# Optimization experiments

Measured on AMD Instinct MI355X. Metric: run time of the kernel, lower is better.

Reference implementation:

```python
import jax, jax.numpy as jnp
import numpy as np

NDIM = (256, 256, 256)
NMIN = (-1.0, -1.0, -1.0)
NMAX = (1.0, 1.0, 1.0)
NDELTA = tuple((NMAX[i] - NMIN[i]) / (NDIM[i] - 1.0) for i in range(3))
MIN_DEG, MAX_DEG = 0, 10
ANNEALED_ALPHA = 1.0
EPS = 1e-12


def compute_grad(grid):
    # central differences on the voxel grid with edge padding -> [N, 3]
    g = grid.reshape(NDIM[0], NDIM[1], NDIM[2])
    p = jnp.pad(g, ((1, 1), (1, 1), (1, 1)), mode='edge')
    dx = (p[2:, 1:-1, 1:-1] - p[:-2, 1:-1, 1:-1]) / (2.0 * NDELTA[0])
    dy = (p[1:-1, 2:, 1:-1] - p[1:-1, :-2, 1:-1]) / (2.0 * NDELTA[1])
    dz = (p[1:-1, 1:-1, 2:] - p[1:-1, 1:-1, :-2]) / (2.0 * NDELTA[2])
    return jnp.stack([dx, dy, dz], axis=-1).reshape(-1, 3)


def trilinear3(data, pts):
    # data: [N, 4] flattened voxel features, pts: [B, 3] -> [B, 4]
    x = (pts[..., 0] - NMIN[0]) / NDELTA[0]
    y = (pts[..., 1] - NMIN[1]) / NDELTA[1]
    z = (pts[..., 2] - NMIN[2]) / NDELTA[2]
    x0f = jnp.floor(x); y0f = jnp.floor(y); z0f = jnp.floor(z)
    xd = (x - x0f)[..., None]
    yd = (y - y0f)[..., None]
    zd = (z - z0f)[..., None]
    x0 = jnp.clip(x0f.astype(jnp.int32), 0, NDIM[0] - 1)
    x1 = jnp.clip(x0f.astype(jnp.int32) + 1, 0, NDIM[0] - 1)
    y0 = jnp.clip(y0f.astype(jnp.int32), 0, NDIM[1] - 1)
    y1 = jnp.clip(y0f.astype(jnp.int32) + 1, 0, NDIM[1] - 1)
    z0 = jnp.clip(z0f.astype(jnp.int32), 0, NDIM[2] - 1)
    z1 = jnp.clip(z0f.astype(jnp.int32) + 1, 0, NDIM[2] - 1)
    sYZ, sZ = NDIM[1] * NDIM[2], NDIM[2]
    gat = lambda i, j, k: data[sYZ * i + sZ * j + k]
    c00 = gat(x0, y0, z0) * (1 - xd) + gat(x1, y0, z0) * xd
    c01 = gat(x0, y0, z1) * (1 - xd) + gat(x1, y0, z1) * xd
    c10 = gat(x0, y1, z0) * (1 - xd) + gat(x1, y1, z0) * xd
    c11 = gat(x0, y1, z1) * (1 - xd) + gat(x1, y1, z1) * xd
    c0 = c00 * (1 - yd) + c10 * yd
    c1 = c01 * (1 - yd) + c11 * yd
    return c0 * (1 - zd) + c1 * zd


def annealed_pos_enc(x, alpha):
    # nerfies-style windowed positional encoding with identity concat
    bands = jnp.arange(MIN_DEG, MAX_DEG, dtype=x.dtype)  # [D]
    scales = 2.0 ** bands
    xb = x[..., None, :] * scales[:, None]               # [..., D, 3]
    four = jnp.sin(jnp.stack([xb, xb + 0.5 * jnp.pi], axis=-2))  # [..., D, 2, 3]
    w = jnp.clip(alpha - bands, 0.0, 1.0)
    w = 0.5 * (1.0 - jnp.cos(jnp.pi * w))                # cosine easing window
    four = four * w[:, None, None]
    four = four.reshape(x.shape[:-1] + (-1,))            # [..., D*6]
    return jnp.concatenate([x, four], axis=-1)           # [..., 3 + D*6]


def mlp(feats, w0, b0, w1, b1, w2, b2, w3, b3, wo, bo):
    # net_depth=4, skip_layer=2 -> concat inputs after layer index 2
    h = jax.nn.relu(feats @ w0 + b0)
    h = jax.nn.relu(h @ w1 + b1)
    h = jax.nn.relu(h @ w2 + b2)
    h = jnp.concatenate([h, feats], axis=-1)
    h = jax.nn.relu(h @ w3 + b3)
    return h @ wo + bo


def safe_l2_norm(v):
    return jnp.sqrt(jnp.sum(v * v, axis=-1, keepdims=True) + EPS)


def setup_inputs() -> dict:
    key = jax.random.key(0)
    ks = jax.random.split(key, 8)
    B = 1048576
    N = NDIM[0] * NDIM[1] * NDIM[2]
    x = jax.random.uniform(ks[0], (B, 3), jnp.float32, -1.0, 1.0)
    grid = jax.random.normal(ks[1], (N, 1), jnp.float32)
    glorot = lambda k, fi, fo: jax.random.normal(k, (fi, fo), jnp.float32) * jnp.sqrt(2.0 / (fi + fo))
    return {
        'x': x, 'grid': grid,
        'w0': glorot(ks[2], 63, 128), 'b0': jnp.zeros((128,), jnp.float32),
        'w1': glorot(ks[3], 128, 128), 'b1': jnp.zeros((128,), jnp.float32),
        'w2': glorot(ks[4], 128, 128), 'b2': jnp.zeros((128,), jnp.float32),
        'w3': glorot(ks[5], 191, 128), 'b3': jnp.zeros((128,), jnp.float32),
        'wo': jax.random.normal(ks[6], (128, 3), jnp.float32) * 1e-5,  # output_init normal(1e-5)
        'bo': jnp.zeros((3,), jnp.float32),
    }


def reference(x, grid, w0, b0, w1, b1, w2, b2, w3, b3, wo, bo):
    data = jnp.concatenate([grid, compute_grad(grid)], axis=-1)  # [N, 4]
    ret = trilinear3(data, x)                                    # [B, 4]
    feats = annealed_pos_enc(x[:, None], ANNEALED_ALPHA * MAX_DEG)  # [B, 1, 63]
    raw = mlp(feats, w0, b0, w1, b1, w2, b2, w3, b3, wo, bo)[:, 0]  # [B, 3]
    # residual + direct output: rotate gradient vector by axis-angle raw
    theta = safe_l2_norm(raw)
    e = raw / theta
    cond = ret[..., 1:]
    a = safe_l2_norm(cond)
    v = cond / a
    rot = a * (jnp.cos(theta) * v + jnp.sin(theta) * jnp.cross(e, v)
               + (1.0 - jnp.cos(theta)) * jnp.sum(e * v, axis=-1, keepdims=True) * e)
    return (ret[..., :1], ret[..., 1:], rot)
```

## Files before the change

### kernel.cpp

```cpp
#include <hip/hip_runtime.h>


typedef __attribute__((ext_vector_type(4))) float f4;
typedef long long llg;

__device__ __forceinline__ float bf2f(unsigned int u) {
    union { float f; unsigned int i; } v; v.i = u << 16; return v.f;
}
__device__ __forceinline__ unsigned int pkbf(float a, float b) {
    unsigned int r;
    asm("v_cvt_pk_bf16_f32 %0, %1, %2" : "=v"(r) : "v"(a), "v"(b));
    return r;
}
__device__ __forceinline__ float gv(const float* __restrict__ g, int i, int j, int k) {
    return g[(i * 256 + j) * 256 + k];
}
__device__ __forceinline__ int featmap(int kp) {
    if (kp < 3) return kp;
    if (kp == 3) return -1;
    const int m = kp - 4, b = m / 6, r = m - 6 * b, d = r >> 1, c = r & 1;
    return 3 + 6 * b + 3 * c + d;
}
__device__ __forceinline__ int hidperm(int k) {
    const int kt = k >> 5, q = (k >> 3) & 3, j = k & 7;
    return 32 * kt + ((j >> 2) << 4) + (q << 2) + (j & 3);
}
__device__ __forceinline__ llg mkllg(unsigned int lo, unsigned int hi) {
    return (llg)(((unsigned long long)lo) | (((unsigned long long)hi) << 32));
}
__device__ __forceinline__ unsigned int pack8(f4 acc) {
    int d = __builtin_amdgcn_cvt_pk_fp8_f32(fmaxf(acc[0], 0.f), fmaxf(acc[1], 0.f), 0, false);
    d     = __builtin_amdgcn_cvt_pk_fp8_f32(fmaxf(acc[2], 0.f), fmaxf(acc[3], 0.f), d, true);
    return (unsigned int)d;
}

#define WS_TOTAL 67584
#define SWZ_BLOCKS 264
#define DG_BLOCKS 8192
#define DG_OFF_SH 131072
#define WS_NEED (262144ull + 16777216ull * 8ull)
#define WO_SCALE 8192.0f
#define WO_INV   (1.0f / 8192.0f)

__global__ __launch_bounds__(256) void prep(
    const float* __restrict__ g,
    const float* __restrict__ w0, const float* __restrict__ w1,
    const float* __restrict__ w2, const float* __restrict__ w3,
    const float* __restrict__ wo,
    unsigned char* __restrict__ ws8, unsigned short* __restrict__ dg,
    int do_dgrid)
{
    const int bid = blockIdx.x;
    if (bid < SWZ_BLOCKS) {
        int idx = bid * 256 + threadIdx.x;
        const float* src; int base, NT, Kact, Nact, ld;
        if (idx < 8192)       { src = w0; base = 0;     NT = 8; Kact = 64;  Nact = 128; ld = 128; }
        else if (idx < 24576) { src = w1; base = 8192;  NT = 8; Kact = 128; Nact = 128; ld = 128; }
        else if (idx < 40960) { src = w2; base = 24576; NT = 8; Kact = 128; Nact = 128; ld = 128; }
        else if (idx < 65536) { src = w3; base = 40960; NT = 8; Kact = 192; Nact = 128; ld = 128; }
        else                  { src = wo; base = 65536; NT = 1; Kact = 128; Nact = 3;   ld = 3;   }
        int local = idx - base;
        int j = local & 7;
        int lane = (local >> 3) & 63;
        int chunk = local >> 9;
        int nt = chunk % NT, kt = chunk / NT;
        int k = kt * 32 + ((lane >> 4) << 3) + j;
        int n = nt * 16 + (lane & 15);
        float v = 0.0f;
        if (k < Kact && n < Nact) {
            int ko;
            if (base == 0) {
                ko = featmap(k);
            } else if (base == 40960) {
                if (k >= 128) {
                    int f = featmap(k - 128);
                    ko = (f < 0) ? -1 : 128 + f;
                } else {
                    ko = hidperm(k);
                }
            } else {
                ko = hidperm(k);
            }
            if (ko >= 0) v = src[ko * ld + n];
            if (base == 65536) v *= WO_SCALE;
        }
        int p = __builtin_amdgcn_cvt_pk_fp8_f32(v, v, 0, false);
        ws8[idx] = (unsigned char)(p & 0xff);
    } else if (do_dgrid) {
        const int t  = (bid - SWZ_BLOCKS) * 256 + threadIdx.x;
        const int k0 = (t & 31) << 3;
        const int j  = (t >> 5) & 255;
        const int i  = t >> 13;
        const float* row = g + (i * 256 + j) * 256;
        const float* rxp = g + (min(i + 1, 255) * 256 + j) * 256;
        const float* rxm = g + (max(i - 1, 0)   * 256 + j) * 256;
        const float* ryp = g + (i * 256 + min(j + 1, 255)) * 256;
        const float* rym = g + (i * 256 + max(j - 1, 0))   * 256;
        float se[8], sxp[8], sxm[8], syp[8], sym[8];
        {
            f4 a = *(const f4*)(row + k0), b = *(const f4*)(row + k0 + 4);
            #pragma unroll
            for (int q = 0; q < 4; ++q) { se[q] = a[q]; se[q + 4] = b[q]; }
            a = *(const f4*)(rxp + k0); b = *(const f4*)(rxp + k0 + 4);
            #pragma unroll
            for (int q = 0; q < 4; ++q) { sxp[q] = a[q]; sxp[q + 4] = b[q]; }
            a = *(const f4*)(rxm + k0); b = *(const f4*)(rxm + k0 + 4);
            #pragma unroll
            for (int q = 0; q < 4; ++q) { sxm[q] = a[q]; sxm[q + 4] = b[q]; }
            a = *(const f4*)(ryp + k0); b = *(const f4*)(ryp + k0 + 4);
            #pragma unroll
            for (int q = 0; q < 4; ++q) { syp[q] = a[q]; syp[q + 4] = b[q]; }
            a = *(const f4*)(rym + k0); b = *(const f4*)(rym + k0 + 4);
            #pragma unroll
            for (int q = 0; q < 4; ++q) { sym[q] = a[q]; sym[q + 4] = b[q]; }
        }
        float zv[10];
        zv[0] = row[max(k0 - 1, 0)];
        #pragma unroll
        for (int q = 0; q < 8; ++q) zv[q + 1] = se[q];
        zv[9] = row[min(k0 + 8, 255)];
        unsigned int o[16];
        #pragma unroll
        for (int q = 0; q < 8; ++q) {
            o[q * 2 + 0] = pkbf(se[q], (sxp[q] - sxm[q]) * 63.75f);
            o[q * 2 + 1] = pkbf((syp[q] - sym[q]) * 63.75f, (zv[q + 2] - zv[q]) * 63.75f);
        }
        unsigned short* dst = dg + (size_t)(((i * 256 + j) * 256 + k0)) * 4;
        #pragma unroll
        for (int q = 0; q < 4; ++q)
            *(uint4*)(dst + q * 8) = *(const uint4*)(&o[q * 4]);
    }
}

#define FSTRIDE_B 88
#define WV_BYTES (32 * FSTRIDE_B)

#define HIDDEN_LAYER(WSL, BIASP, SRC, DST)                                     \
    do {                                                                       \
        _Pragma("unroll")                                                      \
        for (int ut = 0; ut < 8; ++ut) {                                       \
            llg wf0 = *(const llg*)((WSL) + (((0 * 8 + ut) * 64 + lane) << 3));\
            llg wf1 = *(const llg*)((WSL) + (((1 * 8 + ut) * 64 + lane) << 3));\
            llg wf2 = *(const llg*)((WSL) + (((2 * 8 + ut) * 64 + lane) << 3));\
            llg wf3 = *(const llg*)((WSL) + (((3 * 8 + ut) * 64 + lane) << 3));\
            const f4 bias = *(const f4*)((BIASP) + ut * 16 + quad * 4);        \
            _Pragma("unroll")                                                  \
            for (int pt = 0; pt < 2; ++pt) {                                   \
                f4 acc = bias;                                                 \
                acc = __builtin_amdgcn_mfma_f32_16x16x32_fp8_fp8(              \
                        wf0, mkllg(SRC[pt][0], SRC[pt][1]), acc, 0, 0, 0);     \
                acc = __builtin_amdgcn_mfma_f32_16x16x32_fp8_fp8(              \
                        wf1, mkllg(SRC[pt][2], SRC[pt][3]), acc, 0, 0, 0);     \
                acc = __builtin_amdgcn_mfma_f32_16x16x32_fp8_fp8(              \
                        wf2, mkllg(SRC[pt][4], SRC[pt][5]), acc, 0, 0, 0);     \
                acc = __builtin_amdgcn_mfma_f32_16x16x32_fp8_fp8(              \
                        wf3, mkllg(SRC[pt][6], SRC[pt][7]), acc, 0, 0, 0);     \
                DST[pt][ut] = pack8(acc);                                      \
            }                                                                  \
        }                                                                      \
    } while (0)

template<bool FAST>
__global__ __launch_bounds__(256, 5) void voxmlp(
    const float* __restrict__ x, const float* __restrict__ grid,
    const unsigned char* __restrict__ ws8, const unsigned short* __restrict__ dg,
    const float* __restrict__ b0, const float* __restrict__ b1,
    const float* __restrict__ b2, const float* __restrict__ b3,
    const float* __restrict__ bo,
    float* __restrict__ out, int B)
{
    __shared__ unsigned char smem[WV_BYTES * 4];

    const int lane = threadIdx.x & 63;
    const int wave = threadIdx.x >> 6;
    const int quad = lane >> 4;
    const int lm   = lane & 15;
    unsigned char* fbuf = smem + wave * WV_BYTES;

    const int pbase = blockIdx.x * 128 + wave * 32;

    const int p2   = lane & 31;
    const int role = lane >> 5;
    const int pid  = pbase + p2;

    const float px = x[pid * 3 + 0];
    const float py = x[pid * 3 + 1];
    const float pz = x[pid * 3 + 2];

    if (role == 0) {
        const float fx = (px + 1.0f) * 127.5f;
        const float fy = (py + 1.0f) * 127.5f;
        const float fz = (pz + 1.0f) * 127.5f;
        const float fx0 = floorf(fx), fy0 = floorf(fy), fz0 = floorf(fz);
        const float xd = fx - fx0, yd = fy - fy0, zd = fz - fz0;
        const int ix0 = min(max((int)fx0, 0), 255);
        const int iy0 = min(max((int)fy0, 0), 255);
        const int iz0 = min(max((int)fz0, 0), 255);
        const int ix1 = min(ix0 + 1, 255);
        const int iy1 = min(iy0 + 1, 255);
        const int iz1 = min(iz0 + 1, 255);

        float ret0 = 0.f, c1 = 0.f, c2 = 0.f, c3 = 0.f;
        if (FAST) {
            #pragma unroll
            for (int c = 0; c < 8; ++c) {
                const int i = (c & 4) ? ix1 : ix0;
                const int j = (c & 2) ? iy1 : iy0;
                const int k = (c & 1) ? iz1 : iz0;
                const float wgt = ((c & 4) ? xd : 1.0f - xd) *
                                  ((c & 2) ? yd : 1.0f - yd) *
                                  ((c & 1) ? zd : 1.0f - zd);
                const uint2 w = *(const uint2*)(dg + (size_t)((i * 256 + j) * 256 + k) * 4);
                ret0 = fmaf(wgt, bf2f(w.x & 0xffffu), ret0);
                c1   = fmaf(wgt, bf2f(w.x >> 16),     c1);
                c2   = fmaf(wgt, bf2f(w.y & 0xffffu), c2);
                c3   = fmaf(wgt, bf2f(w.y >> 16),     c3);
            }
        } else {
            #pragma unroll
            for (int c = 0; c < 8; ++c) {
                const int i = (c & 4) ? ix1 : ix0;
                const int j = (c & 2) ? iy1 : iy0;
                const int k = (c & 1) ? iz1 : iz0;
                const float wgt = ((c & 4) ? xd : 1.0f - xd) *
                                  ((c & 2) ? yd : 1.0f - yd) *
                                  ((c & 1) ? zd : 1.0f - zd);
                const float v  = gv(grid, i, j, k);
                const float gx = (gv(grid, min(i + 1, 255), j, k) - gv(grid, max(i - 1, 0), j, k)) * 63.75f;
                const float gy = (gv(grid, i, min(j + 1, 255), k) - gv(grid, i, max(j - 1, 0), k)) * 63.75f;
                const float gz = (gv(grid, i, j, min(k + 1, 255)) - gv(grid, i, j, max(k - 1, 0))) * 63.75f;
                ret0 = fmaf(wgt, v,  ret0);
                c1   = fmaf(wgt, gx, c1);
                c2   = fmaf(wgt, gy, c2);
                c3   = fmaf(wgt, gz, c3);
            }
        }
        out[pid] = ret0;
        out[B + pid * 3 + 0] = c1;
        out[B + pid * 3 + 1] = c2;
        out[B + pid * 3 + 2] = c3;
        float* cst = (float*)(fbuf + p2 * FSTRIDE_B + 64);
        cst[0] = c1; cst[1] = c2; cst[2] = c3;
    } else {
        float s[64];
        s[0] = px; s[1] = py; s[2] = pz; s[3] = 0.0f;
        const float crd[3] = {px, py, pz};
        float sc = 1.0f;
        #pragma unroll
        for (int b = 0; b < 10; ++b) {
            #pragma unroll
            for (int d = 0; d < 3; ++d) {
                float sv, cv;
                __sincosf(crd[d] * sc, &sv, &cv);
                s[4 + b * 6 + d * 2 + 0] = sv;
                s[4 + b * 6 + d * 2 + 1] = cv;
            }
            sc *= 2.0f;
        }
        unsigned int dw[16];
        #pragma unroll
        for (int i = 0; i < 16; ++i) {
            int d = __builtin_amdgcn_cvt_pk_fp8_f32(s[4 * i + 0], s[4 * i + 1], 0, false);
            d     = __builtin_amdgcn_cvt_pk_fp8_f32(s[4 * i + 2], s[4 * i + 3], d, true);
            dw[i] = (unsigned int)d;
        }
        unsigned char* fb = fbuf + p2 * FSTRIDE_B;
        #pragma unroll
        for (int i = 0; i < 8; ++i) {
            uint2 pk; pk.x = dw[2 * i]; pk.y = dw[2 * i + 1];
            *(uint2*)(fb + i * 8) = pk;
        }
    }
    __builtin_amdgcn_s_barrier();

    const int frow0 = lm * FSTRIDE_B + quad * 8;

    unsigned int actA[2][8];
    unsigned int actB[2][8];

    {
        llg ff[2][2];
        #pragma unroll
        for (int pt = 0; pt < 2; ++pt)
            #pragma unroll
            for (int kt = 0; kt < 2; ++kt)
                ff[pt][kt] = *(const llg*)(fbuf + pt * 16 * FSTRIDE_B + frow0 + kt * 32);
        #pragma unroll
        for (int ut = 0; ut < 8; ++ut) {
            llg wf0 = *(const llg*)(ws8 + (((0 * 8 + ut) * 64 + lane) << 3));
            llg wf1 = *(const llg*)(ws8 + (((1 * 8 + ut) * 64 + lane) << 3));
            const f4 bias = *(const f4*)(b0 + ut * 16 + quad * 4);
            #pragma unroll
            for (int pt = 0; pt < 2; ++pt) {
                f4 acc = bias;
                acc = __builtin_amdgcn_mfma_f32_16x16x32_fp8_fp8(wf0, ff[pt][0], acc, 0, 0, 0);
                acc = __builtin_amdgcn_mfma_f32_16x16x32_fp8_fp8(wf1, ff[pt][1], acc, 0, 0, 0);
                actA[pt][ut] = pack8(acc);
            }
        }
    }

    HIDDEN_LAYER(ws8 + 8192,  b1, actA, actB);
    HIDDEN_LAYER(ws8 + 24576, b2, actB, actA);

    {
        llg ff[2][2];
        #pragma unroll
        for (int pt = 0; pt < 2; ++pt)
            #pragma unroll
            for (int kk = 0; kk < 2; ++kk)
                ff[pt][kk] = *(const llg*)(fbuf + pt * 16 * FSTRIDE_B + frow0 + kk * 32);
        #pragma unroll
        for (int ut = 0; ut < 8; ++ut) {
            llg wf0 = *(const llg*)(ws8 + 40960 + (((0 * 8 + ut) * 64 + lane) << 3));
            llg wf1 = *(const llg*)(ws8 + 40960 + (((1 * 8 + ut) * 64 + lane) << 3));
            llg wf2 = *(const llg*)(ws8 + 40960 + (((2 * 8 + ut) * 64 + lane) << 3));
            llg wf3 = *(const llg*)(ws8 + 40960 + (((3 * 8 + ut) * 64 + lane) << 3));
            llg wf4 = *(const llg*)(ws8 + 40960 + (((4 * 8 + ut) * 64 + lane) << 3));
            llg wf5 = *(const llg*)(ws8 + 40960 + (((5 * 8 + ut) * 64 + lane) << 3));
            const f4 bias = *(const f4*)(b3 + ut * 16 + quad * 4);
            #pragma unroll
            for (int pt = 0; pt < 2; ++pt) {
                f4 acc = bias;
                acc = __builtin_amdgcn_mfma_f32_16x16x32_fp8_fp8(
                        wf0, mkllg(actA[pt][0], actA[pt][1]), acc, 0, 0, 0);
                acc = __builtin_amdgcn_mfma_f32_16x16x32_fp8_fp8(
                        wf1, mkllg(actA[pt][2], actA[pt][3]), acc, 0, 0, 0);
                acc = __builtin_amdgcn_mfma_f32_16x16x32_fp8_fp8(
                        wf2, mkllg(actA[pt][4], actA[pt][5]), acc, 0, 0, 0);
                acc = __builtin_amdgcn_mfma_f32_16x16x32_fp8_fp8(
                        wf3, mkllg(actA[pt][6], actA[pt][7]), acc, 0, 0, 0);
                acc = __builtin_amdgcn_mfma_f32_16x16x32_fp8_fp8(wf4, ff[pt][0], acc, 0, 0, 0);
                acc = __builtin_amdgcn_mfma_f32_16x16x32_fp8_fp8(wf5, ff[pt][1], acc, 0, 0, 0);
                actB[pt][ut] = pack8(acc);
            }
        }
    }

    llg wf0 = *(const llg*)(ws8 + 65536 + ((0 * 64 + lane) << 3));
    llg wf1 = *(const llg*)(ws8 + 65536 + ((1 * 64 + lane) << 3));
    llg wf2 = *(const llg*)(ws8 + 65536 + ((2 * 64 + lane) << 3));
    llg wf3 = *(const llg*)(ws8 + 65536 + ((3 * 64 + lane) << 3));

    const float bo0 = bo[0], bo1 = bo[1], bo2 = bo[2];
    #pragma unroll
    for (int pt = 0; pt < 2; ++pt) {
        f4 acc = {0.f, 0.f, 0.f, 0.f};
        acc = __builtin_amdgcn_mfma_f32_16x16x32_fp8_fp8(
                wf0, mkllg(actB[pt][0], actB[pt][1]), acc, 0, 0, 0);
        acc = __builtin_amdgcn_mfma_f32_16x16x32_fp8_fp8(
                wf1, mkllg(actB[pt][2], actB[pt][3]), acc, 0, 0, 0);
        acc = __builtin_amdgcn_mfma_f32_16x16x32_fp8_fp8(
                wf2, mkllg(actB[pt][4], actB[pt][5]), acc, 0, 0, 0);
        acc = __builtin_amdgcn_mfma_f32_16x16x32_fp8_fp8(
                wf3, mkllg(actB[pt][6], actB[pt][7]), acc, 0, 0, 0);

        const int pp = pt * 16 + lm;
        const float* cst = (const float*)(fbuf + pp * FSTRIDE_B + 64);
        const float g1 = cst[0], g2 = cst[1], g3 = cst[2];
        const float r0 = acc[0] * WO_INV + bo0;
        const float r1 = acc[1] * WO_INV + bo1;
        const float r2 = acc[2] * WO_INV + bo2;
        const float theta = sqrtf(fmaf(r0, r0, fmaf(r1, r1, r2 * r2)) + 1e-12f);
        const float it = __builtin_amdgcn_rcpf(theta);
        const float e0 = r0 * it, e1 = r1 * it, e2 = r2 * it;
        const float a = sqrtf(fmaf(g1, g1, fmaf(g2, g2, g3 * g3)) + 1e-12f);
        const float ia = __builtin_amdgcn_rcpf(a);
        const float v0 = g1 * ia, v1 = g2 * ia, v2 = g3 * ia;
        float st, ct;
        __sincosf(theta, &st, &ct);
        const float cx = e1 * v2 - e2 * v1;
        const float cy = e2 * v0 - e0 * v2;
        const float cz = e0 * v1 - e1 * v0;
        const float om = (1.0f - ct) * (e0 * v0 + e1 * v1 + e2 * v2);
        if (quad == 0) {
            const int pid2 = pbase + pp;
            out[4 * B + pid2 * 3 + 0] = a * (ct * v0 + st * cx + om * e0);
            out[4 * B + pid2 * 3 + 1] = a * (ct * v1 + st * cy + om * e1);
            out[4 * B + pid2 * 3 + 2] = a * (ct * v2 + st * cz + om * e2);
        }
    }
}

extern "C" void kernel_launch(void* const* d_in, const int* in_sizes, int n_in,
                              void* d_out, int out_size, void* d_ws, size_t ws_size,
                              hipStream_t stream)
{
    const float* x    = (const float*)d_in[0];
    const float* grid = (const float*)d_in[1];
    const float* w0   = (const float*)d_in[2];
    const float* b0   = (const float*)d_in[3];
    const float* w1   = (const float*)d_in[4];
    const float* b1   = (const float*)d_in[5];
    const float* w2   = (const float*)d_in[6];
    const float* b2   = (const float*)d_in[7];
    const float* w3   = (const float*)d_in[8];
    const float* b3   = (const float*)d_in[9];
    const float* wo   = (const float*)d_in[10];
    const float* bo   = (const float*)d_in[11];
    float* out = (float*)d_out;
    unsigned char* ws8 = (unsigned char*)d_ws;
    unsigned short* dg = (unsigned short*)d_ws + DG_OFF_SH;

    const int B = in_sizes[0] / 3;
    const int fast = (ws_size >= WS_NEED) ? 1 : 0;
    const int nprep = fast ? (SWZ_BLOCKS + DG_BLOCKS) : SWZ_BLOCKS;
    prep<<<nprep, 256, 0, stream>>>(grid, w0, w1, w2, w3, wo, ws8, dg, fast);
    if (fast)
        voxmlp<true><<<B / 128, 256, 0, stream>>>(x, grid, ws8, dg, b0, b1, b2, b3, bo, out, B);
    else
        voxmlp<false><<<B / 128, 256, 0, stream>>>(x, grid, ws8, dg, b0, b1, b2, b3, bo, out, B);
}
```

Before: 363.7 us.

## Widen weight fragment loads to 16 bytes and use native sin for positional encoding

The prep kernel's weight swizzle now interleaves pairs of K-tiles, so each lane fetches two MFMA fragments with one 16-byte load instead of two 8-byte loads. Output tiles are processed in pairs, with activations kept as packed 64-bit values. The positional encoding uses v_fract plus v_sin in revolutions in place of __sincosf. The trilinear gather computes byte offsets incrementally. The aim is fewer load instructions and less address and transcendental ALU work, at the cost of a layout coupled across both kernels and possibly higher register pressure.

```diff
diff --git a/kernel.cpp b/kernel.cpp
--- a/kernel.cpp
+++ b/kernel.cpp
@@ -3,6 +3,9 @@
 
 typedef __attribute__((ext_vector_type(4))) float f4;
 typedef long long llg;
+typedef __attribute__((ext_vector_type(2))) long long llg2;
+
+#define MFMA8 __builtin_amdgcn_mfma_f32_16x16x32_fp8_fp8
 
 __device__ __forceinline__ float bf2f(unsigned int u) {
     union { float f; unsigned int i; } v; v.i = u << 16; return v.f;
@@ -11,6 +14,12 @@
     unsigned int r;
     asm("v_cvt_pk_bf16_f32 %0, %1, %2" : "=v"(r) : "v"(a), "v"(b));
     return r;
+}
+__device__ __forceinline__ float vfract(float a) {
+    float d; asm("v_fract_f32 %0, %1" : "=v"(d) : "v"(a)); return d;
+}
+__device__ __forceinline__ float vsin(float a) {
+    float d; asm("v_sin_f32 %0, %1" : "=v"(d) : "v"(a)); return d;
 }
 __device__ __forceinline__ float gv(const float* __restrict__ g, int i, int j, int k) {
     return g[(i * 256 + j) * 256 + k];
@@ -53,17 +62,19 @@
     const int bid = blockIdx.x;
     if (bid < SWZ_BLOCKS) {
         int idx = bid * 256 + threadIdx.x;
-        const float* src; int base, NT, Kact, Nact, ld;
-        if (idx < 8192)       { src = w0; base = 0;     NT = 8; Kact = 64;  Nact = 128; ld = 128; }
-        else if (idx < 24576) { src = w1; base = 8192;  NT = 8; Kact = 128; Nact = 128; ld = 128; }
-        else if (idx < 40960) { src = w2; base = 24576; NT = 8; Kact = 128; Nact = 128; ld = 128; }
-        else if (idx < 65536) { src = w3; base = 40960; NT = 8; Kact = 192; Nact = 128; ld = 128; }
-        else                  { src = wo; base = 65536; NT = 1; Kact = 128; Nact = 3;   ld = 3;   }
+        const float* src; int base, KTP, Kact, Nact, ld;
+        if (idx < 8192)       { src = w0; base = 0;     KTP = 1; Kact = 64;  Nact = 128; ld = 128; }
+        else if (idx < 24576) { src = w1; base = 8192;  KTP = 2; Kact = 128; Nact = 128; ld = 128; }
+        else if (idx < 40960) { src = w2; base = 24576; KTP = 2; Kact = 128; Nact = 128; ld = 128; }
+        else if (idx < 65536) { src = w3; base = 40960; KTP = 3; Kact = 192; Nact = 128; ld = 128; }
+        else                  { src = wo; base = 65536; KTP = 2; Kact = 128; Nact = 3;   ld = 3;   }
         int local = idx - base;
-        int j = local & 7;
-        int lane = (local >> 3) & 63;
-        int chunk = local >> 9;
-        int nt = chunk % NT, kt = chunk / NT;
+        int j    = local & 7;
+        int half = (local >> 3) & 1;
+        int lane = (local >> 4) & 63;
+        int c    = local >> 10;
+        int ktp  = c % KTP, nt = c / KTP;
+        int kt   = ktp * 2 + half;
         int k = kt * 32 + ((lane >> 4) << 3) + j;
         int n = nt * 16 + (lane & 15);
         float v = 0.0f;
@@ -135,29 +146,31 @@
 #define FSTRIDE_B 88
 #define WV_BYTES (32 * FSTRIDE_B)
 
-#define HIDDEN_LAYER(WSL, BIASP, SRC, DST)                                     \
-    do {                                                                       \
-        _Pragma("unroll")                                                      \
-        for (int ut = 0; ut < 8; ++ut) {                                       \
-            llg wf0 = *(const llg*)((WSL) + (((0 * 8 + ut) * 64 + lane) << 3));\
-            llg wf1 = *(const llg*)((WSL) + (((1 * 8 + ut) * 64 + lane) << 3));\
-            llg wf2 = *(const llg*)((WSL) + (((2 * 8 + ut) * 64 + lane) << 3));\
-            llg wf3 = *(const llg*)((WSL) + (((3 * 8 + ut) * 64 + lane) << 3));\
-            const f4 bias = *(const f4*)((BIASP) + ut * 16 + quad * 4);        \
-            _Pragma("unroll")                                                  \
-            for (int pt = 0; pt < 2; ++pt) {                                   \
-                f4 acc = bias;                                                 \
-                acc = __builtin_amdgcn_mfma_f32_16x16x32_fp8_fp8(              \
-                        wf0, mkllg(SRC[pt][0], SRC[pt][1]), acc, 0, 0, 0);     \
-                acc = __builtin_amdgcn_mfma_f32_16x16x32_fp8_fp8(              \
-                        wf1, mkllg(SRC[pt][2], SRC[pt][3]), acc, 0, 0, 0);     \
-                acc = __builtin_amdgcn_mfma_f32_16x16x32_fp8_fp8(              \
-                        wf2, mkllg(SRC[pt][4], SRC[pt][5]), acc, 0, 0, 0);     \
-                acc = __builtin_amdgcn_mfma_f32_16x16x32_fp8_fp8(              \
-                        wf3, mkllg(SRC[pt][6], SRC[pt][7]), acc, 0, 0, 0);     \
-                DST[pt][ut] = pack8(acc);                                      \
-            }                                                                  \
-        }                                                                      \
+#define HIDDEN_LAYER(WSL, BIASP, SRCP, DSTP)                                    \
+    do {                                                                        \
+        _Pragma("unroll")                                                       \
+        for (int utp = 0; utp < 4; ++utp) {                                     \
+            const int utA = 2 * utp, utB = 2 * utp + 1;                         \
+            llg2 wa0 = *(const llg2*)((WSL) + ((utA * 2 + 0) * 64 + lane) * 16);\
+            llg2 wa1 = *(const llg2*)((WSL) + ((utA * 2 + 1) * 64 + lane) * 16);\
+            llg2 wb0 = *(const llg2*)((WSL) + ((utB * 2 + 0) * 64 + lane) * 16);\
+            llg2 wb1 = *(const llg2*)((WSL) + ((utB * 2 + 1) * 64 + lane) * 16);\
+            const f4 biasA = *(const f4*)((BIASP) + utA * 16 + quad * 4);       \
+            const f4 biasB = *(const f4*)((BIASP) + utB * 16 + quad * 4);       \
+            _Pragma("unroll")                                                   \
+            for (int pt = 0; pt < 2; ++pt) {                                    \
+                f4 a0 = biasA, a1 = biasB;                                      \
+                a0 = MFMA8(wa0[0], SRCP[pt][0], a0, 0, 0, 0);                   \
+                a0 = MFMA8(wa0[1], SRCP[pt][1], a0, 0, 0, 0);                   \
+                a0 = MFMA8(wa1[0], SRCP[pt][2], a0, 0, 0, 0);                   \
+                a0 = MFMA8(wa1[1], SRCP[pt][3], a0, 0, 0, 0);                   \
+                a1 = MFMA8(wb0[0], SRCP[pt][0], a1, 0, 0, 0);                   \
+                a1 = MFMA8(wb0[1], SRCP[pt][1], a1, 0, 0, 0);                   \
+                a1 = MFMA8(wb1[0], SRCP[pt][2], a1, 0, 0, 0);                   \
+                a1 = MFMA8(wb1[1], SRCP[pt][3], a1, 0, 0, 0);                   \
+                DSTP[pt][utp] = mkllg(pack8(a0), pack8(a1));                    \
+            }                                                                   \
+        }                                                                       \
     } while (0)
 
 template<bool FAST>
@@ -202,15 +215,20 @@
 
         float ret0 = 0.f, c1 = 0.f, c2 = 0.f, c3 = 0.f;
         if (FAST) {
+            const unsigned char* dgb = (const unsigned char*)dg;
+            const unsigned int vbase = (unsigned int)((ix0 * 65536 + iy0 * 256 + iz0) << 3);
+            const unsigned int ox = (unsigned int)((ix1 - ix0) << 19);
+            const unsigned int oy = (unsigned int)((iy1 - iy0) << 11);
+            const unsigned int oz = (unsigned int)((iz1 - iz0) << 3);
             #pragma unroll
             for (int c = 0; c < 8; ++c) {
-                const int i = (c & 4) ? ix1 : ix0;
-                const int j = (c & 2) ? iy1 : iy0;
-                const int k = (c & 1) ? iz1 : iz0;
                 const float wgt = ((c & 4) ? xd : 1.0f - xd) *
                                   ((c & 2) ? yd : 1.0f - yd) *
                                   ((c & 1) ? zd : 1.0f - zd);
-                const uint2 w = *(const uint2*)(dg + (size_t)((i * 256 + j) * 256 + k) * 4);
+                const unsigned int off = vbase + ((c & 4) ? ox : 0u)
+                                               + ((c & 2) ? oy : 0u)
+                                               + ((c & 1) ? oz : 0u);
+                const uint2 w = *(const uint2*)(dgb + off);
                 ret0 = fmaf(wgt, bf2f(w.x & 0xffffu), ret0);
                 c1   = fmaf(wgt, bf2f(w.x >> 16),     c1);
                 c2   = fmaf(wgt, bf2f(w.y & 0xffffu), c2);
@@ -244,18 +262,18 @@
     } else {
         float s[64];
         s[0] = px; s[1] = py; s[2] = pz; s[3] = 0.0f;
-        const float crd[3] = {px, py, pz};
-        float sc = 1.0f;
+        float r0 = px * 0.15915494309189535f;
+        float r1 = py * 0.15915494309189535f;
+        float r2 = pz * 0.15915494309189535f;
         #pragma unroll
         for (int b = 0; b < 10; ++b) {
-            #pragma unroll
-            for (int d = 0; d < 3; ++d) {
-                float sv, cv;
-                __sincosf(crd[d] * sc, &sv, &cv);
-                s[4 + b * 6 + d * 2 + 0] = sv;
-                s[4 + b * 6 + d * 2 + 1] = cv;
-            }
-            sc *= 2.0f;
+            s[4 + b * 6 + 0] = vsin(vfract(r0));
+            s[4 + b * 6 + 1] = vsin(vfract(r0 + 0.25f));
+            s[4 + b * 6 + 2] = vsin(vfract(r1));
+            s[4 + b * 6 + 3] = vsin(vfract(r1 + 0.25f));
+            s[4 + b * 6 + 4] = vsin(vfract(r2));
+            s[4 + b * 6 + 5] = vsin(vfract(r2 + 0.25f));
+            r0 += r0; r1 += r1; r2 += r2;
         }
         unsigned int dw[16];
         #pragma unroll
@@ -275,85 +293,79 @@
 
     const int frow0 = lm * FSTRIDE_B + quad * 8;
 
-    unsigned int actA[2][8];
-    unsigned int actB[2][8];
-
-    {
-        llg ff[2][2];
-        #pragma unroll
-        for (int pt = 0; pt < 2; ++pt)
-            #pragma unroll
-            for (int kt = 0; kt < 2; ++kt)
-                ff[pt][kt] = *(const llg*)(fbuf + pt * 16 * FSTRIDE_B + frow0 + kt * 32);
-        #pragma unroll
-        for (int ut = 0; ut < 8; ++ut) {
-            llg wf0 = *(const llg*)(ws8 + (((0 * 8 + ut) * 64 + lane) << 3));
-            llg wf1 = *(const llg*)(ws8 + (((1 * 8 + ut) * 64 + lane) << 3));
-            const f4 bias = *(const f4*)(b0 + ut * 16 + quad * 4);
-            #pragma unroll
-            for (int pt = 0; pt < 2; ++pt) {
-                f4 acc = bias;
-                acc = __builtin_amdgcn_mfma_f32_16x16x32_fp8_fp8(wf0, ff[pt][0], acc, 0, 0, 0);
-                acc = __builtin_amdgcn_mfma_f32_16x16x32_fp8_fp8(wf1, ff[pt][1], acc, 0, 0, 0);
-                actA[pt][ut] = pack8(acc);
-            }
+    llg actA[2][4];
+    llg actB[2][4];
+    llg ffp[2][2];
+
+    #pragma unroll
+    for (int pt = 0; pt < 2; ++pt)
+        #pragma unroll
+        for (int kt = 0; kt < 2; ++kt)
+            ffp[pt][kt] = *(const llg*)(fbuf + pt * 16 * FSTRIDE_B + frow0 + kt * 32);
+
+    #pragma unroll
+    for (int utp = 0; utp < 4; ++utp) {
+        const int utA = 2 * utp, utB = 2 * utp + 1;
+        llg2 wA = *(const llg2*)(ws8 + (utA * 64 + lane) * 16);
+        llg2 wB = *(const llg2*)(ws8 + (utB * 64 + lane) * 16);
+        const f4 biasA = *(const f4*)(b0 + utA * 16 + quad * 4);
+        const f4 biasB = *(const f4*)(b0 + utB * 16 + quad * 4);
+        #pragma unroll
+        for (int pt = 0; pt < 2; ++pt) {
+            f4 a0 = biasA, a1 = biasB;
+            a0 = MFMA8(wA[0], ffp[pt][0], a0, 0, 0, 0);
+            a0 = MFMA8(wA[1], ffp[pt][1], a0, 0, 0, 0);
+            a1 = MFMA8(wB[0], ffp[pt][0], a1, 0, 0, 0);
+            a1 = MFMA8(wB[1], ffp[pt][1], a1, 0, 0, 0);
+            actA[pt][utp] = mkllg(pack8(a0), pack8(a1));
         }
     }
 
     HIDDEN_LAYER(ws8 + 8192,  b1, actA, actB);
     HIDDEN_LAYER(ws8 + 24576, b2, actB, actA);
 
-    {
-        llg ff[2][2];
-        #pragma unroll
-        for (int pt = 0; pt < 2; ++pt)
-            #pragma unroll
-            for (int kk = 0; kk < 2; ++kk)
-                ff[pt][kk] = *(const llg*)(fbuf + pt * 16 * FSTRIDE_B + frow0 + kk * 32);
-        #pragma unroll
-        for (int ut = 0; ut < 8; ++ut) {
-            llg wf0 = *(const llg*)(ws8 + 40960 + (((0 * 8 + ut) * 64 + lane) << 3));
-            llg wf1 = *(const llg*)(ws8 + 40960 + (((1 * 8 + ut) * 64 + lane) << 3));
-            llg wf2 = *(const llg*)(ws8 + 40960 + (((2 * 8 + ut) * 64 + lane) << 3));
-            llg wf3 = *(const llg*)(ws8 + 40960 + (((3 * 8 + ut) * 64 + lane) << 3));
-            llg wf4 = *(const llg*)(ws8 + 40960 + (((4 * 8 + ut) * 64 + lane) << 3));
-            llg wf5 = *(const llg*)(ws8 + 40960 + (((5 * 8 + ut) * 64 + lane) << 3));
-            const f4 bias = *(const f4*)(b3 + ut * 16 + quad * 4);
-            #pragma unroll
-            for (int pt = 0; pt < 2; ++pt) {
-                f4 acc = bias;
-                acc = __builtin_amdgcn_mfma_f32_16x16x32_fp8_fp8(
-                        wf0, mkllg(actA[pt][0], actA[pt][1]), acc, 0, 0, 0);
-                acc = __builtin_amdgcn_mfma_f32_16x16x32_fp8_fp8(
-                        wf1, mkllg(actA[pt][2], actA[pt][3]), acc, 0, 0, 0);
-                acc = __builtin_amdgcn_mfma_f32_16x16x32_fp8_fp8(
-                        wf2, mkllg(actA[pt][4], actA[pt][5]), acc, 0, 0, 0);
-                acc = __builtin_amdgcn_mfma_f32_16x16x32_fp8_fp8(
-                        wf3, mkllg(actA[pt][6], actA[pt][7]), acc, 0, 0, 0);
-                acc = __builtin_amdgcn_mfma_f32_16x16x32_fp8_fp8(wf4, ff[pt][0], acc, 0, 0, 0);
-                acc = __builtin_amdgcn_mfma_f32_16x16x32_fp8_fp8(wf5, ff[pt][1], acc, 0, 0, 0);
-                actB[pt][ut] = pack8(acc);
-            }
+    #pragma unroll
+    for (int utp = 0; utp < 4; ++utp) {
+        const int utA = 2 * utp, utB = 2 * utp + 1;
+        llg2 ha0 = *(const llg2*)(ws8 + 40960 + ((utA * 3 + 0) * 64 + lane) * 16);
+        llg2 ha1 = *(const llg2*)(ws8 + 40960 + ((utA * 3 + 1) * 64 + lane) * 16);
+        llg2 ha2 = *(const llg2*)(ws8 + 40960 + ((utA * 3 + 2) * 64 + lane) * 16);
+        llg2 hb0 = *(const llg2*)(ws8 + 40960 + ((utB * 3 + 0) * 64 + lane) * 16);
+        llg2 hb1 = *(const llg2*)(ws8 + 40960 + ((utB * 3 + 1) * 64 + lane) * 16);
+        llg2 hb2 = *(const llg2*)(ws8 + 40960 + ((utB * 3 + 2) * 64 + lane) * 16);
+        const f4 biasA = *(const f4*)(b3 + utA * 16 + quad * 4);
+        const f4 biasB = *(const f4*)(b3 + utB * 16 + quad * 4);
+        #pragma unroll
+        for (int pt = 0; pt < 2; ++pt) {
+            f4 a0 = biasA, a1 = biasB;
+            a0 = MFMA8(ha0[0], actA[pt][0], a0, 0, 0, 0);
+            a0 = MFMA8(ha0[1], actA[pt][1], a0, 0, 0, 0);
+            a0 = MFMA8(ha1[0], actA[pt][2], a0, 0, 0, 0);
+            a0 = MFMA8(ha1[1], actA[pt][3], a0, 0, 0, 0);
+            a0 = MFMA8(ha2[0], ffp[pt][0],  a0, 0, 0, 0);
+            a0 = MFMA8(ha2[1], ffp[pt][1],  a0, 0, 0, 0);
+            a1 = MFMA8(hb0[0], actA[pt][0], a1, 0, 0, 0);
+            a1 = MFMA8(hb0[1], actA[pt][1], a1, 0, 0, 0);
+            a1 = MFMA8(hb1[0], actA[pt][2], a1, 0, 0, 0);
+            a1 = MFMA8(hb1[1], actA[pt][3], a1, 0, 0, 0);
+            a1 = MFMA8(hb2[0], ffp[pt][0],  a1, 0, 0, 0);
+            a1 = MFMA8(hb2[1], ffp[pt][1],  a1, 0, 0, 0);
+            actB[pt][utp] = mkllg(pack8(a0), pack8(a1));
         }
     }
 
-    llg wf0 = *(const llg*)(ws8 + 65536 + ((0 * 64 + lane) << 3));
-    llg wf1 = *(const llg*)(ws8 + 65536 + ((1 * 64 + lane) << 3));
-    llg wf2 = *(const llg*)(ws8 + 65536 + ((2 * 64 + lane) << 3));
-    llg wf3 = *(const llg*)(ws8 + 65536 + ((3 * 64 + lane) << 3));
+    llg2 o0 = *(const llg2*)(ws8 + 65536 + ((0 * 64 + lane) * 16));
+    llg2 o1 = *(const llg2*)(ws8 + 65536 + ((1 * 64 + lane) * 16) + 64 * 16 * 0);
+    o1 = *(const llg2*)(ws8 + 65536 + ((64 + lane) * 16));
 
     const float bo0 = bo[0], bo1 = bo[1], bo2 = bo[2];
     #pragma unroll
     for (int pt = 0; pt < 2; ++pt) {
         f4 acc = {0.f, 0.f, 0.f, 0.f};
-        acc = __builtin_amdgcn_mfma_f32_16x16x32_fp8_fp8(
-                wf0, mkllg(actB[pt][0], actB[pt][1]), acc, 0, 0, 0);
-        acc = __builtin_amdgcn_mfma_f32_16x16x32_fp8_fp8(
-                wf1, mkllg(actB[pt][2], actB[pt][3]), acc, 0, 0, 0);
-        acc = __builtin_amdgcn_mfma_f32_16x16x32_fp8_fp8(
-                wf2, mkllg(actB[pt][4], actB[pt][5]), acc, 0, 0, 0);
-        acc = __builtin_amdgcn_mfma_f32_16x16x32_fp8_fp8(
-                wf3, mkllg(actB[pt][6], actB[pt][7]), acc, 0, 0, 0);
+        acc = MFMA8(o0[0], actB[pt][0], acc, 0, 0, 0);
+        acc = MFMA8(o0[1], actB[pt][1], acc, 0, 0, 0);
+        acc = MFMA8(o1[0], actB[pt][2], acc, 0, 0, 0);
+        acc = MFMA8(o1[1], actB[pt][3], acc, 0, 0, 0);
 
         const int pp = pt * 16 + lm;
         const float* cst = (const float*)(fbuf + pp * FSTRIDE_B + 64);
```

New measurement: 335.4 us. -7.8%, faster.
